# Kernel optimization log

Measured on AMD Instinct MI355X. Metric: run time of the kernel, lower is better.

Reference implementation:

```python
import jax, jax.numpy as jnp
import numpy as np

N = 50000      # total nodes in batched graph
E = 800000     # total edges (avg degree 16)
B = 512        # number of graphs in batch
F_IN = 74      # input node feature size
H = 64         # hidden size per layer
OUT = 64       # output_feats
EPS = 1e-5     # BatchNorm eps


def setup_inputs() -> dict:
    key = jax.random.key(0)
    ks = jax.random.split(key, 32)
    d = {}
    d['feats'] = jax.random.normal(ks[0], (N, F_IN), dtype=jnp.float32)
    d['src'] = jax.random.randint(ks[1], (E,), 0, N)
    d['dst'] = jax.random.randint(ks[2], (E,), 0, N)
    d['graph_ids'] = jnp.sort(jax.random.randint(ks[3], (N,), 0, B))
    dims = [F_IN, H, H, H]
    i = 4
    for l in range(3):
        din, dout = dims[l], dims[l + 1]
        d[f'W{l}'] = jax.random.normal(ks[i], (din, dout), jnp.float32) / np.sqrt(din).astype(np.float32); i += 1
        d[f'b{l}'] = jnp.zeros((dout,), jnp.float32)
        d[f'rW{l}'] = jax.random.normal(ks[i], (din, dout), jnp.float32) / np.sqrt(din).astype(np.float32); i += 1
        d[f'rb{l}'] = jnp.zeros((dout,), jnp.float32)
        d[f'g{l}'] = jnp.ones((dout,), jnp.float32)    # BN gamma
        d[f'be{l}'] = jnp.zeros((dout,), jnp.float32)  # BN beta
    d['aw_W'] = jax.random.normal(ks[i], (H, 1), jnp.float32) / np.sqrt(H).astype(np.float32); i += 1
    d['aw_b'] = jnp.zeros((1,), jnp.float32)
    d['out_W'] = jax.random.normal(ks[i], (2 * H, OUT), jnp.float32) / np.sqrt(2 * H).astype(np.float32); i += 1
    d['out_b'] = jnp.zeros((OUT,), jnp.float32)
    return d


def _gcn_layer(x, src, dst, W, b, rW, rb, g, be):
    # GraphConv, norm='none': out = sum-aggregate(X W) + b, then relu
    xw = x @ W                                                    # [N, dout]
    agg = jax.ops.segment_sum(xw[src], dst, num_segments=N) + b   # gather/scatter over edges
    h = jax.nn.relu(agg)
    # residual: relu(Linear(x))
    h = h + jax.nn.relu(x @ rW + rb)
    # dropout p=0 -> identity
    # BatchNorm1d (training-mode batch statistics, biased variance)
    mean = jnp.mean(h, axis=0)
    var = jnp.var(h, axis=0)
    return (h - mean) * jax.lax.rsqrt(var + EPS) * g + be


def reference(feats, src, dst, graph_ids,
              W0, b0, rW0, rb0, g0, be0,
              W1, b1, rW1, rb1, g1, be1,
              W2, b2, rW2, rb2, g2, be2,
              aw_W, aw_b, out_W, out_b):
    h = feats
    h = _gcn_layer(h, src, dst, W0, b0, rW0, rb0, g0, be0)
    h = _gcn_layer(h, src, dst, W1, b1, rW1, rb1, g1, be1)
    h = _gcn_layer(h, src, dst, W2, b2, rW2, rb2, g2, be2)
    # WeightedSumAndMax readout
    w = jax.nn.sigmoid(h @ aw_W + aw_b)                               # [N, 1]
    h_sum = jax.ops.segment_sum(h * w, graph_ids, num_segments=B)     # [B, H]
    h_max = jax.ops.segment_max(h, graph_ids, num_segments=B)         # [B, H]
    h_max = jnp.where(jnp.isfinite(h_max), h_max, 0.0)                # empty graphs -> 0 (dgl max_nodes)
    h_g = jnp.concatenate([h_sum, h_max], axis=1)                     # [B, 2H]
    return h_g @ out_W + out_b                                        # [B, OUT]
```

## Files before the change

kernel.cpp:

```cpp
#include <hip/hip_runtime.h>
#include <hip/hip_bf16.h>
#include <math.h>

#define NN 50000
#define NE 800000
#define NB 512
#define FIN 74
#define HD 64
#define BN_EPS 1e-5f

#define SCHUNK 512
#define NCHUNK ((NN + SCHUNK - 1) / SCHUNK)

#define CHUNK 32
#define ELLW 32
#define NBLK ((NN + CHUNK - 1) / CHUNK)


__global__ void csr_zero_kernel(int* __restrict__ cnt, int* __restrict__ cnt2,
                                float* __restrict__ stats012,
                                unsigned long long* __restrict__ xw_zrow,
                                const float* __restrict__ W0, const float* __restrict__ rW0,
                                float2* __restrict__ Wpk0) {
    int i = blockIdx.x * 256 + threadIdx.x;
    if (i < NN) { cnt[i] = 0; cnt2[i] = 0; }
    if (i < 384) stats012[i] = 0.f;
    if (i < 16) xw_zrow[i] = 0ull;
    if (i < FIN * HD) Wpk0[i] = make_float2(W0[i], rW0[i]);
}

__global__ void csr_hist_kernel(const int* __restrict__ dst, int* __restrict__ cnt) {
    int e = blockIdx.x * 256 + threadIdx.x;
    if (e < NE) atomicAdd(&cnt[dst[e]], 1);
}

__global__ void scanA_kernel(const int* __restrict__ cnt, int* __restrict__ bsum) {
    __shared__ int l[SCHUNK];
    int i = blockIdx.x * SCHUNK + threadIdx.x;
    int v = (i < NN) ? cnt[i] : 0;
    l[threadIdx.x] = v;
    __syncthreads();
    for (int off = SCHUNK / 2; off; off >>= 1) {
        if (threadIdx.x < off) l[threadIdx.x] += l[threadIdx.x + off];
        __syncthreads();
    }
    if (threadIdx.x == 0) bsum[blockIdx.x] = l[0];
}

__global__ void scanB_kernel(int* __restrict__ bsum) {
    int lane = threadIdx.x;
    int v0 = (lane < NCHUNK) ? bsum[lane] : 0;
    int v1 = (64 + lane < NCHUNK) ? bsum[64 + lane] : 0;
    int s0 = v0, s1 = v1;
    for (int off = 1; off < 64; off <<= 1) {
        int t0 = __shfl_up(s0, off, 64);
        int t1 = __shfl_up(s1, off, 64);
        if (lane >= off) { s0 += t0; s1 += t1; }
    }
    int tot0 = __shfl(s0, 63, 64);
    if (lane < NCHUNK) bsum[lane] = s0 - v0;
    if (64 + lane < NCHUNK) bsum[64 + lane] = s1 - v1 + tot0;
}

__global__ void scanC_kernel(const int* __restrict__ cnt, const int* __restrict__ bsum,
                             int* __restrict__ row_ptr) {
    __shared__ int l[SCHUNK];
    int i = blockIdx.x * SCHUNK + threadIdx.x;
    int v = (i < NN) ? cnt[i] : 0;
    l[threadIdx.x] = v;
    __syncthreads();
    for (int off = 1; off < SCHUNK; off <<= 1) {
        int t = (threadIdx.x >= off) ? l[threadIdx.x - off] : 0;
        __syncthreads();
        l[threadIdx.x] += t;
        __syncthreads();
    }
    int excl = l[threadIdx.x] - v + bsum[blockIdx.x];
    if (i < NN) row_ptr[i] = excl;
    if (i == NN - 1) row_ptr[NN] = excl + v;
}

__global__ void csr_fill_kernel(const int* __restrict__ src, const int* __restrict__ dst,
                                const int* __restrict__ row_ptr, int* __restrict__ cnt2,
                                int* __restrict__ eidx) {
    int i = blockIdx.x * 256 + threadIdx.x;
    if (i < NE) {
        int d = dst[i];
        int p = row_ptr[d] + atomicAdd(&cnt2[d], 1);
        eidx[p] = src[i];
    }
}


template <int K>
__global__ __launch_bounds__(256) void gemm_dual_kernel(
    const float* __restrict__ x, const float2* __restrict__ Wpk,
    const float* __restrict__ rb, __hip_bfloat16* __restrict__ xw,
    __hip_bfloat16* __restrict__ res, int n) {
    __shared__ float2 sW[K * HD];
    __shared__ float srb[64];
    for (int i = threadIdx.x; i < K * HD; i += 256) sW[i] = Wpk[i];
    if (threadIdx.x < 64) srb[threadIdx.x] = rb[threadIdx.x];
    __syncthreads();
    int wl = threadIdx.x >> 6, lane = threadIdx.x & 63;
    for (int r0 = (blockIdx.x * 4 + wl) * 8; r0 < n; r0 += gridDim.x * 32) {
        float a1[8], a2[8];
#pragma unroll
        for (int r = 0; r < 8; ++r) { a1[r] = 0.f; a2[r] = 0.f; }
#pragma unroll
        for (int c0 = 0; c0 < K; c0 += 64) {
            const int cl = (K - c0 < 64) ? (K - c0) : 64;
            float xv[8];
#pragma unroll
            for (int r = 0; r < 8; ++r) {
                int row = r0 + r;
                xv[r] = (lane < cl && row < n) ? x[(size_t)row * K + c0 + lane] : 0.f;
            }
            for (int j = 0; j < cl; ++j) {
                float2 w = sW[(c0 + j) * HD + lane];
#pragma unroll
                for (int r = 0; r < 8; ++r) {
                    float xb = __uint_as_float(
                        __builtin_amdgcn_readlane(__float_as_uint(xv[r]), j));
                    a1[r] = fmaf(xb, w.x, a1[r]);
                    a2[r] = fmaf(xb, w.y, a2[r]);
                }
            }
        }
#pragma unroll
        for (int r = 0; r < 8; ++r) {
            int row = r0 + r;
            if (row < n) {
                xw[(size_t)row * HD + lane] = __float2bfloat16(a1[r]);
                res[(size_t)row * HD + lane] = __float2bfloat16(fmaxf(a2[r] + srb[lane], 0.f));
            }
        }
    }
}

__global__ void fold_kernel(const float* __restrict__ stats, const float* __restrict__ g,
                            const float* __restrict__ be, const float* __restrict__ W,
                            const float* __restrict__ rW, const float* __restrict__ rb,
                            float2* __restrict__ Wpk, float* __restrict__ shiftW,
                            float* __restrict__ rbp) {
    __shared__ float sc[64], sh[64];
    int t = threadIdx.x;
    if (t < 64) {
        float mean = stats[t] / (float)NN;
        float var = stats[64 + t] / (float)NN - mean * mean;
        float scale = g[t] * rsqrtf(var + BN_EPS);
        sc[t] = scale;
        sh[t] = be[t] - mean * scale;
    }
    __syncthreads();
    for (int i = t; i < 64 * 64; i += 256) {
        int k = i >> 6;
        Wpk[i] = make_float2(sc[k] * W[i], sc[k] * rW[i]);
    }
    if (t < 64) {
        float sw = 0.f, srw = 0.f;
        for (int k = 0; k < 64; ++k) {
            sw = fmaf(sh[k], W[k * 64 + t], sw);
            srw = fmaf(sh[k], rW[k * 64 + t], srw);
        }
        shiftW[t] = sw;
        rbp[t] = rb[t] + srw;
    }
}

__device__ __forceinline__ float bf_lo(unsigned int p) { return __uint_as_float(p << 16); }
__device__ __forceinline__ float bf_hi(unsigned int p) { return __uint_as_float(p & 0xffff0000u); }

#define GATHER16(BASE)                                             \
    {                                                              \
        unsigned long long d[16];                                  \
        _Pragma("unroll") for (int j = 0; j < 16; ++j) {           \
            int idx = sIdx[rloc][(BASE) + j];                      \
            unsigned off = (unsigned)idx * 16u + (unsigned)c8;     \
            d[j] = XWu[off];                                       \
        }                                                          \
        _Pragma("unroll") for (int j = 0; j < 16; ++j) {           \
            unsigned lo = (unsigned)d[j], hi = (unsigned)(d[j] >> 32); \
            a0 += bf_lo(lo); a1 += bf_hi(lo);                      \
            a2 += bf_lo(hi); a3 += bf_hi(hi);                      \
        }                                                          \
    }

__global__ __launch_bounds__(256, 4) void fused_agg_kernel(
    const __hip_bfloat16* __restrict__ xw, const __hip_bfloat16* __restrict__ res,
    const float* __restrict__ b, const float* __restrict__ shiftW,
    const int* __restrict__ row_ptr, const int* __restrict__ geidx,
    float* __restrict__ hout, float* __restrict__ stats, int n) {
    __shared__ int sIdx[CHUNK][ELLW + 1];
    __shared__ int sRP[CHUNK + 1];
    __shared__ int sLen[CHUNK];
    __shared__ float sbb[128];
    __shared__ float lsr[4][16][8];

    int tid = threadIdx.x;
    int r0 = blockIdx.x * CHUNK;

    if (tid <= CHUNK) {
        int rp = r0 + tid;
        sRP[tid] = row_ptr[(rp < NN) ? rp : NN];
    }
    if (tid >= 128 && tid < 256) {
        int j = tid - 128;
        sbb[j] = (j < 64) ? b[j] : (shiftW ? shiftW[j - 64] : 0.f);
    }
    __syncthreads();
    for (int i = tid; i < CHUNK * ELLW; i += 256) {
        int r = i >> 5, j = i & 31;
        int beg = sRP[r];
        int plen = sRP[r + 1] - beg;
        sIdx[r][j] = (j < plen) ? geidx[beg + j] : NN;
        if (j == 0) sLen[r] = plen;
    }
    __syncthreads();

    const unsigned long long* XWu = (const unsigned long long*)xw;
    const unsigned long long* REu = (const unsigned long long*)res;
    int wl = tid >> 6, lane = tid & 63;
    int q = lane >> 4, c8 = lane & 15;
    float sb0 = sbb[4 * c8], sb1 = sbb[4 * c8 + 1], sb2 = sbb[4 * c8 + 2], sb3 = sbb[4 * c8 + 3];
    float sw0 = sbb[64 + 4 * c8], sw1 = sbb[64 + 4 * c8 + 1];
    float sw2 = sbb[64 + 4 * c8 + 2], sw3 = sbb[64 + 4 * c8 + 3];
    float s0 = 0.f, s1 = 0.f, s2 = 0.f, s3 = 0.f;
    float q0 = 0.f, q1 = 0.f, q2 = 0.f, q3 = 0.f;

#pragma unroll
    for (int p = 0; p < 2; ++p) {
        int rbase = wl * 8 + p * 4;
        int rloc = rbase + q;
        int grow = r0 + rloc;
        int growc = (grow < n) ? grow : (n - 1);
        int l0 = sLen[rbase], l1 = sLen[rbase + 1], l2 = sLen[rbase + 2], l3 = sLen[rbase + 3];
        int m01 = (l0 > l1) ? l0 : l1, m23 = (l2 > l3) ? l2 : l3;
        int kmax = (m01 > m23) ? m01 : m23;
        int mylen = sLen[rloc];
        unsigned long long rqw = REu[(unsigned)growc * 16u + (unsigned)c8];
        float a0 = 0.f, a1 = 0.f, a2 = 0.f, a3 = 0.f;
        GATHER16(0)
        if (kmax > 16) GATHER16(16)
        if (kmax > ELLW) {
            int beg = sRP[rloc];
            for (int k = ELLW; k < kmax; ++k) {
                int idx = geidx[beg + k];
                unsigned off = (unsigned)((k < mylen) ? idx : NN) * 16u + (unsigned)c8;
                unsigned long long u = XWu[off];
                unsigned lo = (unsigned)u, hi = (unsigned)(u >> 32);
                a0 += bf_lo(lo); a1 += bf_hi(lo);
                a2 += bf_lo(hi); a3 += bf_hi(hi);
            }
        }
        unsigned rlo = (unsigned)rqw, rhi = (unsigned)(rqw >> 32);
        float dg = (float)mylen;
        float h0 = fmaxf(a0 + fmaf(dg, sw0, sb0), 0.f) + bf_lo(rlo);
        float h1 = fmaxf(a1 + fmaf(dg, sw1, sb1), 0.f) + bf_hi(rlo);
        float h2 = fmaxf(a2 + fmaf(dg, sw2, sb2), 0.f) + bf_lo(rhi);
        float h3 = fmaxf(a3 + fmaf(dg, sw3, sb3), 0.f) + bf_hi(rhi);
        if (grow < n) {
            *(float4*)&hout[(unsigned)grow * 64u + 4u * c8] = make_float4(h0, h1, h2, h3);
            s0 += h0; s1 += h1; s2 += h2; s3 += h3;
            q0 += h0 * h0; q1 += h1 * h1; q2 += h2 * h2; q3 += h3 * h3;
        }
    }

    s0 += __shfl_xor(s0, 16, 64); s0 += __shfl_xor(s0, 32, 64);
    s1 += __shfl_xor(s1, 16, 64); s1 += __shfl_xor(s1, 32, 64);
    s2 += __shfl_xor(s2, 16, 64); s2 += __shfl_xor(s2, 32, 64);
    s3 += __shfl_xor(s3, 16, 64); s3 += __shfl_xor(s3, 32, 64);
    q0 += __shfl_xor(q0, 16, 64); q0 += __shfl_xor(q0, 32, 64);
    q1 += __shfl_xor(q1, 16, 64); q1 += __shfl_xor(q1, 32, 64);
    q2 += __shfl_xor(q2, 16, 64); q2 += __shfl_xor(q2, 32, 64);
    q3 += __shfl_xor(q3, 16, 64); q3 += __shfl_xor(q3, 32, 64);
    if (q == 0) {
        lsr[wl][c8][0] = s0; lsr[wl][c8][1] = s1; lsr[wl][c8][2] = s2; lsr[wl][c8][3] = s3;
        lsr[wl][c8][4] = q0; lsr[wl][c8][5] = q1; lsr[wl][c8][6] = q2; lsr[wl][c8][7] = q3;
    }
    __syncthreads();
    if (tid < 64) {
        int c8i = tid >> 2, comp = tid & 3;
        float ssum = lsr[0][c8i][comp] + lsr[1][c8i][comp] + lsr[2][c8i][comp] + lsr[3][c8i][comp];
        float qsum = lsr[0][c8i][4 + comp] + lsr[1][c8i][4 + comp] + lsr[2][c8i][4 + comp] +
                     lsr[3][c8i][4 + comp];
        atomicAdd(&stats[tid], ssum);
        atomicAdd(&stats[64 + tid], qsum);
    }
}


__global__ void readout_init_kernel(float* __restrict__ hsum, unsigned int* __restrict__ hmax,
                                    const float* __restrict__ stats, const float* __restrict__ g,
                                    const float* __restrict__ be, float* __restrict__ ss) {
    int idx = blockIdx.x * 256 + threadIdx.x;
    if (idx < NB * HD) {
        hsum[idx] = 0.f;
        hmax[idx] = 0x007FFFFFu;
    }
    if (blockIdx.x == 0 && threadIdx.x < 64) {
        int c = threadIdx.x;
        float mean = stats[c] / (float)NN;
        float var = stats[64 + c] / (float)NN - mean * mean;
        float scale = g[c] * rsqrtf(var + BN_EPS);
        ss[c] = scale;
        ss[64 + c] = be[c] - mean * scale;
    }
}

#define RNODES 16

__device__ __forceinline__ void ro_flush(float* hsum, unsigned int* hmax, int g, int c,
                                         float accS, float accM) {
    atomicAdd(&hsum[g * HD + c], accS);
    unsigned int bits = __float_as_uint(accM);
    unsigned int enc = (bits & 0x80000000u) ? ~bits : (bits | 0x80000000u);
    atomicMax(&hmax[g * HD + c], enc);
}

__global__ __launch_bounds__(256) void readout_kernel(
    const float* __restrict__ h, const int* __restrict__ gid, const float* __restrict__ ss,
    const float* __restrict__ awW, const float* __restrict__ awb, float* __restrict__ hsum,
    unsigned int* __restrict__ hmax, int n) {
    int wid = blockIdx.x * 4 + (threadIdx.x >> 6);
    int c = threadIdx.x & 63;
    int r0 = wid * RNODES;
    if (r0 >= n) return;
    int r1 = r0 + RNODES;
    if (r1 > n) r1 = n;
    float aw = awW[c], ab = awb[0];
    float sA = ss[c], sB = ss[64 + c];
    int cur = gid[r0];
    float accS = 0.f, accM = -__builtin_inff();
    for (int r = r0; r < r1; ++r) {
        int g = gid[r];
        if (g != cur) {
            ro_flush(hsum, hmax, cur, c, accS, accM);
            accS = 0.f;
            accM = -__builtin_inff();
            cur = g;
        }
        float v = fmaf(h[(size_t)r * HD + c], sA, sB);
        float p = v * aw;
        for (int off = 32; off; off >>= 1) p += __shfl_xor(p, off, 64);
        float w = 1.f / (1.f + expf(-(p + ab)));
        accS = fmaf(v, w, accS);
        accM = fmaxf(accM, v);
    }
    ro_flush(hsum, hmax, cur, c, accS, accM);
}

__global__ void final_kernel(const float* __restrict__ hsum, const unsigned int* __restrict__ hmax,
                             const float* __restrict__ outW, const float* __restrict__ outb,
                             float* __restrict__ out) {
    __shared__ float sW[128 * 64];
    for (int i = threadIdx.x; i < 128 * 64; i += 256) sW[i] = outW[i];
    __syncthreads();
    int idx = blockIdx.x * 256 + threadIdx.x;
    if (idx >= NB * HD) return;
    int bi = idx >> 6, o = idx & 63;
    float acc = outb[o];
#pragma unroll 4
    for (int k = 0; k < 64; ++k) acc = fmaf(hsum[bi * 64 + k], sW[k * 64 + o], acc);
#pragma unroll 4
    for (int k = 0; k < 64; ++k) {
        unsigned int e = hmax[bi * 64 + k];
        float m;
        if (e == 0x007FFFFFu) {
            m = 0.f;
        } else {
            m = (e & 0x80000000u) ? __uint_as_float(e ^ 0x80000000u) : __uint_as_float(~e);
        }
        acc = fmaf(m, sW[(64 + k) * 64 + o], acc);
    }
    out[idx] = acc;
}


extern "C" void kernel_launch(void* const* d_in, const int* in_sizes, int n_in,
                              void* d_out, int out_size, void* d_ws, size_t ws_size,
                              hipStream_t stream) {
    const float* feats = (const float*)d_in[0];
    const int* src = (const int*)d_in[1];
    const int* dst = (const int*)d_in[2];
    const int* gid = (const int*)d_in[3];
    const float* W[3];
    const float* b[3];
    const float* rW[3];
    const float* rb[3];
    const float* g[3];
    const float* be[3];
    for (int l = 0; l < 3; ++l) {
        W[l] = (const float*)d_in[4 + 6 * l + 0];
        b[l] = (const float*)d_in[4 + 6 * l + 1];
        rW[l] = (const float*)d_in[4 + 6 * l + 2];
        rb[l] = (const float*)d_in[4 + 6 * l + 3];
        g[l] = (const float*)d_in[4 + 6 * l + 4];
        be[l] = (const float*)d_in[4 + 6 * l + 5];
    }
    const float* awW = (const float*)d_in[22];
    const float* awb = (const float*)d_in[23];
    const float* outW = (const float*)d_in[24];
    const float* outb = (const float*)d_in[25];
    float* out = (float*)d_out;

    __hip_bfloat16* XW = (__hip_bfloat16*)d_ws;
    __hip_bfloat16* RES = XW + (size_t)(NN + 1) * HD;
    float* P1 = (float*)(RES + (size_t)NN * HD);
    float* stats = P1 + (size_t)NN * HD;
    float* ss2 = stats + 384;
    float2* WPK = (float2*)(ss2 + 128);
    float* shW = (float*)(WPK + FIN * HD);
    float* rbp = shW + 64;
    float* hsum = rbp + 64;
    unsigned int* hmax = (unsigned int*)(hsum + (size_t)NB * HD);
    int* cnt = (int*)(hmax + (size_t)NB * HD);
    int* cnt2 = cnt + NN;
    int* row_ptr = cnt2 + NN;
    int* bsum = row_ptr + NN + 1;
    int* eidx = bsum + NCHUNK;

    float* stats0 = stats;
    float* stats1 = stats + 128;
    float* stats2 = stats + 256;

    const int EBLK = (NE + 255) / 256;
    const int GEMMBLK = 1280;
    const int ROBLK = (NN + RNODES * 4 - 1) / (RNODES * 4);

    csr_zero_kernel<<<(NN + 255) / 256, 256, 0, stream>>>(
        cnt, cnt2, stats, (unsigned long long*)(XW + (size_t)NN * HD), W[0], rW[0], WPK);
    csr_hist_kernel<<<EBLK, 256, 0, stream>>>(dst, cnt);
    scanA_kernel<<<NCHUNK, SCHUNK, 0, stream>>>(cnt, bsum);
    scanB_kernel<<<1, 64, 0, stream>>>(bsum);
    scanC_kernel<<<NCHUNK, SCHUNK, 0, stream>>>(cnt, bsum, row_ptr);
    csr_fill_kernel<<<EBLK, 256, 0, stream>>>(src, dst, row_ptr, cnt2, eidx);

    gemm_dual_kernel<FIN><<<GEMMBLK, 256, 0, stream>>>(feats, WPK, rb[0], XW, RES, NN);
    fused_agg_kernel<<<NBLK, 256, 0, stream>>>(XW, RES, b[0], (const float*)nullptr, row_ptr,
                                               eidx, P1, stats0, NN);

    fold_kernel<<<1, 256, 0, stream>>>(stats0, g[0], be[0], W[1], rW[1], rb[1], WPK, shW, rbp);
    gemm_dual_kernel<HD><<<GEMMBLK, 256, 0, stream>>>(P1, WPK, rbp, XW, RES, NN);
    fused_agg_kernel<<<NBLK, 256, 0, stream>>>(XW, RES, b[1], shW, row_ptr, eidx, P1, stats1, NN);

    fold_kernel<<<1, 256, 0, stream>>>(stats1, g[1], be[1], W[2], rW[2], rb[2], WPK, shW, rbp);
    gemm_dual_kernel<HD><<<GEMMBLK, 256, 0, stream>>>(P1, WPK, rbp, XW, RES, NN);
    fused_agg_kernel<<<NBLK, 256, 0, stream>>>(XW, RES, b[2], shW, row_ptr, eidx, P1, stats2, NN);

    readout_init_kernel<<<(NB * HD + 255) / 256, 256, 0, stream>>>(hsum, hmax, stats2, g[2], be[2], ss2);
    readout_kernel<<<ROBLK, 256, 0, stream>>>(P1, gid, ss2, awW, awb, hsum, hmax, NN);
    final_kernel<<<(NB * HD + 255) / 256, 256, 0, stream>>>(hsum, hmax, outW, outb, out);
}
```

Before: 371.2 us.

## Build CSR via two-pass bucketed scatter with shared-memory local fill

Replaces the single-pass CSR fill, which did a global per-node atomic and a random scatter for every edge, with two passes. The first scatters (src,dst) pairs into 64-row buckets using one atomic per bucket. The second has one block per bucket place each edge into its final slot using shared-memory atomics. This is meant to improve write locality and reduce contention on global atomics, at the cost of an extra pass and an 8-byte-per-edge pairs buffer in the workspace.

```diff
diff --git a/kernel.cpp b/kernel.cpp
--- a/kernel.cpp
+++ b/kernel.cpp
@@ -16,14 +16,18 @@
 #define ELLW 32
 #define NBLK ((NN + CHUNK - 1) / CHUNK)
 
-
-__global__ void csr_zero_kernel(int* __restrict__ cnt, int* __restrict__ cnt2,
+#define BROWS 64
+#define NBUCK ((NN + BROWS - 1) / BROWS)
+
+
+__global__ void csr_zero_kernel(int* __restrict__ cnt, int* __restrict__ bcnt,
                                 float* __restrict__ stats012,
                                 unsigned long long* __restrict__ xw_zrow,
                                 const float* __restrict__ W0, const float* __restrict__ rW0,
                                 float2* __restrict__ Wpk0) {
     int i = blockIdx.x * 256 + threadIdx.x;
-    if (i < NN) { cnt[i] = 0; cnt2[i] = 0; }
+    if (i < NN) cnt[i] = 0;
+    if (i < NBUCK) bcnt[i] = 0;
     if (i < 384) stats012[i] = 0.f;
     if (i < 16) xw_zrow[i] = 0ull;
     if (i < FIN * HD) Wpk0[i] = make_float2(W0[i], rW0[i]);
@@ -80,14 +84,38 @@
     if (i == NN - 1) row_ptr[NN] = excl + v;
 }
 
-__global__ void csr_fill_kernel(const int* __restrict__ src, const int* __restrict__ dst,
-                                const int* __restrict__ row_ptr, int* __restrict__ cnt2,
-                                int* __restrict__ eidx) {
-    int i = blockIdx.x * 256 + threadIdx.x;
-    if (i < NE) {
-        int d = dst[i];
-        int p = row_ptr[d] + atomicAdd(&cnt2[d], 1);
-        eidx[p] = src[i];
+__global__ void bucket_scatter_kernel(const int* __restrict__ src, const int* __restrict__ dst,
+                                      const int* __restrict__ row_ptr, int* __restrict__ bcnt,
+                                      int2* __restrict__ pairs) {
+    int e = blockIdx.x * 256 + threadIdx.x;
+    if (e < NE) {
+        int d = dst[e];
+        int bk = d >> 6;
+        int base = row_ptr[bk << 6];
+        int p = base + atomicAdd(&bcnt[bk], 1);
+        pairs[p] = make_int2(src[e], d);
+    }
+}
+
+__global__ void bucket_fill_kernel(const int2* __restrict__ pairs,
+                                   const int* __restrict__ row_ptr, int* __restrict__ eidx) {
+    __shared__ int lcnt[BROWS];
+    __shared__ int sRPb[BROWS + 1];
+    int bk = blockIdx.x;
+    int rbase = bk * BROWS;
+    int tid = threadIdx.x;
+    if (tid <= BROWS) {
+        int rp = rbase + tid;
+        sRPb[tid] = row_ptr[(rp < NN) ? rp : NN];
+    }
+    if (tid < BROWS) lcnt[tid] = 0;
+    __syncthreads();
+    int beg = sRPb[0], end = sRPb[BROWS];
+    for (int i = beg + tid; i < end; i += 256) {
+        int2 pr = pairs[i];
+        int r = pr.y - rbase;
+        int ls = atomicAdd(&lcnt[r], 1);
+        eidx[sRPb[r] + ls] = pr.x;
     }
 }
 
@@ -414,11 +442,12 @@
     float* rbp = shW + 64;
     float* hsum = rbp + 64;
     unsigned int* hmax = (unsigned int*)(hsum + (size_t)NB * HD);
-    int* cnt = (int*)(hmax + (size_t)NB * HD);
-    int* cnt2 = cnt + NN;
-    int* row_ptr = cnt2 + NN;
+    int2* pairs = (int2*)(hmax + (size_t)NB * HD);
+    int* cnt = (int*)(pairs + (size_t)NE);
+    int* row_ptr = cnt + NN;
     int* bsum = row_ptr + NN + 1;
-    int* eidx = bsum + NCHUNK;
+    int* bcnt = bsum + NCHUNK;
+    int* eidx = bcnt + NBUCK;
 
     float* stats0 = stats;
     float* stats1 = stats + 128;
@@ -429,12 +458,13 @@
     const int ROBLK = (NN + RNODES * 4 - 1) / (RNODES * 4);
 
     csr_zero_kernel<<<(NN + 255) / 256, 256, 0, stream>>>(
-        cnt, cnt2, stats, (unsigned long long*)(XW + (size_t)NN * HD), W[0], rW[0], WPK);
+        cnt, bcnt, stats, (unsigned long long*)(XW + (size_t)NN * HD), W[0], rW[0], WPK);
     csr_hist_kernel<<<EBLK, 256, 0, stream>>>(dst, cnt);
     scanA_kernel<<<NCHUNK, SCHUNK, 0, stream>>>(cnt, bsum);
     scanB_kernel<<<1, 64, 0, stream>>>(bsum);
     scanC_kernel<<<NCHUNK, SCHUNK, 0, stream>>>(cnt, bsum, row_ptr);
-    csr_fill_kernel<<<EBLK, 256, 0, stream>>>(src, dst, row_ptr, cnt2, eidx);
+    bucket_scatter_kernel<<<EBLK, 256, 0, stream>>>(src, dst, row_ptr, bcnt, pairs);
+    bucket_fill_kernel<<<NBUCK, 256, 0, stream>>>(pairs, row_ptr, eidx);
 
     gemm_dual_kernel<FIN><<<GEMMBLK, 256, 0, stream>>>(feats, WPK, rb[0], XW, RES, NN);
     fused_agg_kernel<<<NBLK, 256, 0, stream>>>(XW, RES, b[0], (const float*)nullptr, row_ptr,
```

Measured after the change: 522.6 us. 1.41x slower.

## Replace per-node CSR build with 32-node bucket sort and in-block row assembly

Applied to the files above, without the earlier changes.

Replaces the per-node histogram/scan/fill CSR construction with a coarse bucket sort keyed on 32-node chunks. Edges are packed as (src, local-row) pairs and built from per-block shared-memory histograms plus a two-level scan. Each aggregation block then distributes its bucket's pairs into shared-memory ELL rows with shared atomics and spills rows longer than 32 into an overflow list. This removes the global atomics on 50k counters and several scan kernels. The cost is redoing the shared-memory row assembly in all three layers, nondeterministic summation order, and silently dropping edges if overflow exceeds 512 per block.

```diff
diff --git a/kernel.cpp b/kernel.cpp
--- a/kernel.cpp
+++ b/kernel.cpp
@@ -9,85 +9,98 @@
 #define HD 64
 #define BN_EPS 1e-5f
 
-#define SCHUNK 512
-#define NCHUNK ((NN + SCHUNK - 1) / SCHUNK)
-
 #define CHUNK 32
 #define ELLW 32
 #define NBLK ((NN + CHUNK - 1) / CHUNK)
-
-
-__global__ void csr_zero_kernel(int* __restrict__ cnt, int* __restrict__ cnt2,
-                                float* __restrict__ stats012,
-                                unsigned long long* __restrict__ xw_zrow,
-                                const float* __restrict__ W0, const float* __restrict__ rW0,
-                                float2* __restrict__ Wpk0) {
+#define NBUCK2 NBLK
+#define EB2 128
+#define EPB (NE / EB2)
+#define OCAP 512
+
+
+__global__ void init_kernel(float* __restrict__ stats012,
+                            unsigned long long* __restrict__ xw_zrow,
+                            const float* __restrict__ W0, const float* __restrict__ rW0,
+                            float2* __restrict__ Wpk0) {
     int i = blockIdx.x * 256 + threadIdx.x;
-    if (i < NN) { cnt[i] = 0; cnt2[i] = 0; }
     if (i < 384) stats012[i] = 0.f;
     if (i < 16) xw_zrow[i] = 0ull;
     if (i < FIN * HD) Wpk0[i] = make_float2(W0[i], rW0[i]);
 }
 
-__global__ void csr_hist_kernel(const int* __restrict__ dst, int* __restrict__ cnt) {
-    int e = blockIdx.x * 256 + threadIdx.x;
-    if (e < NE) atomicAdd(&cnt[dst[e]], 1);
-}
-
-__global__ void scanA_kernel(const int* __restrict__ cnt, int* __restrict__ bsum) {
-    __shared__ int l[SCHUNK];
-    int i = blockIdx.x * SCHUNK + threadIdx.x;
-    int v = (i < NN) ? cnt[i] : 0;
-    l[threadIdx.x] = v;
-    __syncthreads();
-    for (int off = SCHUNK / 2; off; off >>= 1) {
-        if (threadIdx.x < off) l[threadIdx.x] += l[threadIdx.x + off];
+__global__ __launch_bounds__(256) void hist2_kernel(const int* __restrict__ dst,
+                                                    int* __restrict__ H) {
+    __shared__ int lh[NBUCK2];
+    int b = blockIdx.x, tid = threadIdx.x;
+    for (int i = tid; i < NBUCK2; i += 256) lh[i] = 0;
+    __syncthreads();
+    int e0 = b * EPB;
+    for (int i = tid; i < EPB; i += 256) atomicAdd(&lh[dst[e0 + i] >> 5], 1);
+    __syncthreads();
+    for (int i = tid; i < NBUCK2; i += 256) H[b * NBUCK2 + i] = lh[i];
+}
+
+__global__ __launch_bounds__(128) void scanA2_kernel(int* __restrict__ H, int* __restrict__ T) {
+    __shared__ int l[128];
+    int k = blockIdx.x, tid = threadIdx.x;
+    int v = H[tid * NBUCK2 + k];
+    l[tid] = v;
+    __syncthreads();
+    for (int off = 1; off < 128; off <<= 1) {
+        int t = (tid >= off) ? l[tid - off] : 0;
         __syncthreads();
-    }
-    if (threadIdx.x == 0) bsum[blockIdx.x] = l[0];
-}
-
-__global__ void scanB_kernel(int* __restrict__ bsum) {
-    int lane = threadIdx.x;
-    int v0 = (lane < NCHUNK) ? bsum[lane] : 0;
-    int v1 = (64 + lane < NCHUNK) ? bsum[64 + lane] : 0;
-    int s0 = v0, s1 = v1;
-    for (int off = 1; off < 64; off <<= 1) {
-        int t0 = __shfl_up(s0, off, 64);
-        int t1 = __shfl_up(s1, off, 64);
-        if (lane >= off) { s0 += t0; s1 += t1; }
-    }
-    int tot0 = __shfl(s0, 63, 64);
-    if (lane < NCHUNK) bsum[lane] = s0 - v0;
-    if (64 + lane < NCHUNK) bsum[64 + lane] = s1 - v1 + tot0;
-}
-
-__global__ void scanC_kernel(const int* __restrict__ cnt, const int* __restrict__ bsum,
-                             int* __restrict__ row_ptr) {
-    __shared__ int l[SCHUNK];
-    int i = blockIdx.x * SCHUNK + threadIdx.x;
-    int v = (i < NN) ? cnt[i] : 0;
-    l[threadIdx.x] = v;
-    __syncthreads();
-    for (int off = 1; off < SCHUNK; off <<= 1) {
-        int t = (threadIdx.x >= off) ? l[threadIdx.x - off] : 0;
+        l[tid] += t;
         __syncthreads();
-        l[threadIdx.x] += t;
+    }
+    H[tid * NBUCK2 + k] = l[tid] - v;
+    if (tid == 127) T[k] = l[127];
+}
+
+__global__ __launch_bounds__(256) void scanB2_kernel(const int* __restrict__ T,
+                                                     int* __restrict__ bbase) {
+    __shared__ int l[256];
+    __shared__ int carry;
+    int tid = threadIdx.x;
+    if (tid == 0) carry = 0;
+    __syncthreads();
+    for (int c0 = 0; c0 < NBUCK2; c0 += 256) {
+        int v = (c0 + tid < NBUCK2) ? T[c0 + tid] : 0;
+        l[tid] = v;
         __syncthreads();
-    }
-    int excl = l[threadIdx.x] - v + bsum[blockIdx.x];
-    if (i < NN) row_ptr[i] = excl;
-    if (i == NN - 1) row_ptr[NN] = excl + v;
-}
-
-__global__ void csr_fill_kernel(const int* __restrict__ src, const int* __restrict__ dst,
-                                const int* __restrict__ row_ptr, int* __restrict__ cnt2,
-                                int* __restrict__ eidx) {
-    int i = blockIdx.x * 256 + threadIdx.x;
-    if (i < NE) {
-        int d = dst[i];
-        int p = row_ptr[d] + atomicAdd(&cnt2[d], 1);
-        eidx[p] = src[i];
+        for (int off = 1; off < 256; off <<= 1) {
+            int t = (tid >= off) ? l[tid - off] : 0;
+            __syncthreads();
+            l[tid] += t;
+            __syncthreads();
+        }
+        if (c0 + tid < NBUCK2) bbase[c0 + tid] = l[tid] - v + carry;
+        __syncthreads();
+        if (tid == 0) carry += l[255];
+        __syncthreads();
+    }
+    if (tid == 0) bbase[NBUCK2] = carry;
+}
+
+__global__ __launch_bounds__(256) void addC_kernel(int* __restrict__ H,
+                                                   const int* __restrict__ bbase) {
+    int b = blockIdx.x;
+    for (int k = threadIdx.x; k < NBUCK2; k += 256) H[b * NBUCK2 + k] += bbase[k];
+}
+
+__global__ __launch_bounds__(256) void scatter2_kernel(const int* __restrict__ src,
+                                                       const int* __restrict__ dst,
+                                                       const int* __restrict__ H,
+                                                       unsigned* __restrict__ pairs) {
+    __shared__ int cur[NBUCK2];
+    int b = blockIdx.x, tid = threadIdx.x;
+    for (int i = tid; i < NBUCK2; i += 256) cur[i] = H[b * NBUCK2 + i];
+    __syncthreads();
+    int e0 = b * EPB;
+    for (int i = tid; i < EPB; i += 256) {
+        int d = dst[e0 + i];
+        int s = src[e0 + i];
+        int pos = atomicAdd(&cur[d >> 5], 1);
+        pairs[pos] = (unsigned)s | ((unsigned)(d & 31) << 17);
     }
 }
 
@@ -189,34 +202,42 @@
 __global__ __launch_bounds__(256, 4) void fused_agg_kernel(
     const __hip_bfloat16* __restrict__ xw, const __hip_bfloat16* __restrict__ res,
     const float* __restrict__ b, const float* __restrict__ shiftW,
-    const int* __restrict__ row_ptr, const int* __restrict__ geidx,
+    const int* __restrict__ bbase, const unsigned* __restrict__ pairs,
     float* __restrict__ hout, float* __restrict__ stats, int n) {
     __shared__ int sIdx[CHUNK][ELLW + 1];
-    __shared__ int sRP[CHUNK + 1];
     __shared__ int sLen[CHUNK];
+    __shared__ unsigned oflow[OCAP];
+    __shared__ int ocnt;
+    __shared__ int sBB[2];
     __shared__ float sbb[128];
     __shared__ float lsr[4][16][8];
 
     int tid = threadIdx.x;
     int r0 = blockIdx.x * CHUNK;
 
-    if (tid <= CHUNK) {
-        int rp = r0 + tid;
-        sRP[tid] = row_ptr[(rp < NN) ? rp : NN];
-    }
+    for (int i = tid; i < CHUNK * (ELLW + 1); i += 256) ((int*)sIdx)[i] = NN;
+    if (tid < CHUNK) sLen[tid] = 0;
+    if (tid == 0) ocnt = 0;
+    if (tid < 2) sBB[tid] = bbase[blockIdx.x + tid];
     if (tid >= 128 && tid < 256) {
         int j = tid - 128;
         sbb[j] = (j < 64) ? b[j] : (shiftW ? shiftW[j - 64] : 0.f);
     }
     __syncthreads();
-    for (int i = tid; i < CHUNK * ELLW; i += 256) {
-        int r = i >> 5, j = i & 31;
-        int beg = sRP[r];
-        int plen = sRP[r + 1] - beg;
-        sIdx[r][j] = (j < plen) ? geidx[beg + j] : NN;
-        if (j == 0) sLen[r] = plen;
-    }
-    __syncthreads();
+    int beg = sBB[0], end = sBB[1];
+    for (int i = beg + tid; i < end; i += 256) {
+        unsigned v = pairs[i];
+        int rloc = (int)(v >> 17);
+        int rk = atomicAdd(&sLen[rloc], 1);
+        if (rk < ELLW) {
+            sIdx[rloc][rk] = (int)(v & 0x1FFFFu);
+        } else {
+            int o = atomicAdd(&ocnt, 1);
+            if (o < OCAP) oflow[o] = v;
+        }
+    }
+    __syncthreads();
+    int noflow = (ocnt < OCAP) ? ocnt : OCAP;
 
     const unsigned long long* XWu = (const unsigned long long*)xw;
     const unsigned long long* REu = (const unsigned long long*)res;
@@ -243,14 +264,15 @@
         GATHER16(0)
         if (kmax > 16) GATHER16(16)
         if (kmax > ELLW) {
-            int beg = sRP[rloc];
-            for (int k = ELLW; k < kmax; ++k) {
-                int idx = geidx[beg + k];
-                unsigned off = (unsigned)((k < mylen) ? idx : NN) * 16u + (unsigned)c8;
-                unsigned long long u = XWu[off];
-                unsigned lo = (unsigned)u, hi = (unsigned)(u >> 32);
-                a0 += bf_lo(lo); a1 += bf_hi(lo);
-                a2 += bf_lo(hi); a3 += bf_hi(hi);
+            for (int o = 0; o < noflow; ++o) {
+                unsigned v = oflow[o];
+                if ((int)(v >> 17) == rloc) {
+                    unsigned off = (v & 0x1FFFFu) * 16u + (unsigned)c8;
+                    unsigned long long u = XWu[off];
+                    unsigned lo = (unsigned)u, hi = (unsigned)(u >> 32);
+                    a0 += bf_lo(lo); a1 += bf_hi(lo);
+                    a2 += bf_lo(hi); a3 += bf_hi(hi);
+                }
             }
         }
         unsigned rlo = (unsigned)rqw, rhi = (unsigned)(rqw >> 32);
@@ -414,39 +436,37 @@
     float* rbp = shW + 64;
     float* hsum = rbp + 64;
     unsigned int* hmax = (unsigned int*)(hsum + (size_t)NB * HD);
-    int* cnt = (int*)(hmax + (size_t)NB * HD);
-    int* cnt2 = cnt + NN;
-    int* row_ptr = cnt2 + NN;
-    int* bsum = row_ptr + NN + 1;
-    int* eidx = bsum + NCHUNK;
+    unsigned* pairs = (unsigned*)(hmax + (size_t)NB * HD);
+    int* H = (int*)(pairs + (size_t)NE);
+    int* T = H + (size_t)EB2 * NBUCK2;
+    int* bbase = T + NBUCK2;
 
     float* stats0 = stats;
     float* stats1 = stats + 128;
     float* stats2 = stats + 256;
 
-    const int EBLK = (NE + 255) / 256;
     const int GEMMBLK = 1280;
     const int ROBLK = (NN + RNODES * 4 - 1) / (RNODES * 4);
 
-    csr_zero_kernel<<<(NN + 255) / 256, 256, 0, stream>>>(
-        cnt, cnt2, stats, (unsigned long long*)(XW + (size_t)NN * HD), W[0], rW[0], WPK);
-    csr_hist_kernel<<<EBLK, 256, 0, stream>>>(dst, cnt);
-    scanA_kernel<<<NCHUNK, SCHUNK, 0, stream>>>(cnt, bsum);
-    scanB_kernel<<<1, 64, 0, stream>>>(bsum);
-    scanC_kernel<<<NCHUNK, SCHUNK, 0, stream>>>(cnt, bsum, row_ptr);
-    csr_fill_kernel<<<EBLK, 256, 0, stream>>>(src, dst, row_ptr, cnt2, eidx);
+    init_kernel<<<(FIN * HD + 255) / 256, 256, 0, stream>>>(
+        stats, (unsigned long long*)(XW + (size_t)NN * HD), W[0], rW[0], WPK);
+    hist2_kernel<<<EB2, 256, 0, stream>>>(dst, H);
+    scanA2_kernel<<<NBUCK2, 128, 0, stream>>>(H, T);
+    scanB2_kernel<<<1, 256, 0, stream>>>(T, bbase);
+    addC_kernel<<<EB2, 256, 0, stream>>>(H, bbase);
+    scatter2_kernel<<<EB2, 256, 0, stream>>>(src, dst, H, pairs);
 
     gemm_dual_kernel<FIN><<<GEMMBLK, 256, 0, stream>>>(feats, WPK, rb[0], XW, RES, NN);
-    fused_agg_kernel<<<NBLK, 256, 0, stream>>>(XW, RES, b[0], (const float*)nullptr, row_ptr,
-                                               eidx, P1, stats0, NN);
+    fused_agg_kernel<<<NBLK, 256, 0, stream>>>(XW, RES, b[0], (const float*)nullptr, bbase,
+                                               pairs, P1, stats0, NN);
 
     fold_kernel<<<1, 256, 0, stream>>>(stats0, g[0], be[0], W[1], rW[1], rb[1], WPK, shW, rbp);
     gemm_dual_kernel<HD><<<GEMMBLK, 256, 0, stream>>>(P1, WPK, rbp, XW, RES, NN);
-    fused_agg_kernel<<<NBLK, 256, 0, stream>>>(XW, RES, b[1], shW, row_ptr, eidx, P1, stats1, NN);
+    fused_agg_kernel<<<NBLK, 256, 0, stream>>>(XW, RES, b[1], shW, bbase, pairs, P1, stats1, NN);
 
     fold_kernel<<<1, 256, 0, stream>>>(stats1, g[1], be[1], W[2], rW[2], rb[2], WPK, shW, rbp);
     gemm_dual_kernel<HD><<<GEMMBLK, 256, 0, stream>>>(P1, WPK, rbp, XW, RES, NN);
-    fused_agg_kernel<<<NBLK, 256, 0, stream>>>(XW, RES, b[2], shW, row_ptr, eidx, P1, stats2, NN);
+    fused_agg_kernel<<<NBLK, 256, 0, stream>>>(XW, RES, b[2], shW, bbase, pairs, P1, stats2, NN);
 
     readout_init_kernel<<<(NB * HD + 255) / 256, 256, 0, stream>>>(hsum, hmax, stats2, g[2], be[2], ss2);
     readout_kernel<<<ROBLK, 256, 0, stream>>>(P1, gid, ss2, awW, awb, hsum, hmax, NN);
```

After: 323.0 us. 13.0% less time.
